# Performance work log

Measured on AMD Instinct MI355X. Metric: run time of the kernel, lower is better.

The kernel has to match this reference:

```python
import jax, jax.numpy as jnp
import numpy as np

L, N, E, H, K = 2048, 8, 2048, 8192, 8

def setup_inputs() -> dict:
    key = jax.random.key(0)
    ks = jax.random.split(key, 6)
    return {
        'x': jax.random.normal(ks[0], (L, N, E), dtype=jnp.float32),
        'proj1': jax.random.normal(ks[1], (H, E), dtype=jnp.float32) * 0.02,
        'proj1_bias': jax.random.normal(ks[2], (H,), dtype=jnp.float32) * 0.02,
        'proj2': jax.random.normal(ks[3], (E, H), dtype=jnp.float32) * 0.02,
        'proj2_bias': jax.random.normal(ks[4], (E,), dtype=jnp.float32) * 0.02,
        'gate_w': jax.random.normal(ks[5], (E, K), dtype=jnp.float32),
    }

def reference(x, proj1, proj1_bias, proj2, proj2_bias, gate_w):
    # Gating: top-1 expert per token (argmax over expert affinities).
    # NOTE: in the source, every expert applies the SAME shared proj1/proj2,
    # and recv_from_experts restores the original token order exactly, so the
    # dispatch/combine is a mathematical identity permutation. The forward
    # math is therefore exactly a shared two-layer GELU MLP on all tokens.
    dst = jnp.argmax(jnp.einsum('lne,ek->lnk', x, gate_w), axis=-1)  # [L,N] int, routing ids
    h = jax.nn.gelu(jnp.einsum('lne,he->lnh', x, proj1) + proj1_bias, approximate=False)
    out = jnp.einsum('lnh,eh->lne', h, proj2) + proj2_bias
    del dst  # routing does not affect the output (shared expert weights)
    return out
```

## Files before the change

### kernel.cpp

```cpp
#include <hip/hip_runtime.h>
#include <hip/hip_bf16.h>
#include <cstdint>
#include <cstddef>

typedef __bf16 bf16_t;
typedef __bf16 bf16x4 __attribute__((ext_vector_type(4)));
typedef __bf16 bf16x8 __attribute__((ext_vector_type(8)));
typedef float  f32x4  __attribute__((ext_vector_type(4)));

#define L_DIM 2048
#define N_DIM 8
#define E_DIM 2048
#define H_DIM 8192
#define T_DIM (L_DIM * N_DIM)

__global__ __launch_bounds__(256) void cvt_f32_bf16(const float* __restrict__ in,
                                                    bf16_t* __restrict__ out,
                                                    int n4) {
    int stride = gridDim.x * blockDim.x;
    for (int i = blockIdx.x * blockDim.x + threadIdx.x; i < n4; i += stride) {
        float4 v = *(const float4*)(in + (size_t)i * 4);
        bf16x4 o;
        o[0] = (bf16_t)v.x; o[1] = (bf16_t)v.y;
        o[2] = (bf16_t)v.z; o[3] = (bf16_t)v.w;
        *(bf16x4*)(out + (size_t)i * 4) = o;
    }
}

__device__ __forceinline__ float fast_gelu(float x) {
    float x2 = x * x;
    float w  = x * __builtin_fmaf(0.1029456f, x2, 2.3022618f);
    w = fminf(w, 60.0f);
    float s = __builtin_amdgcn_exp2f(w);
    float r = __builtin_amdgcn_rcpf(s + 1.0f);
    return x * s * r;
}

template <bool GELU_OUT, int LG_NT, int LG_TN, int LG_NTILE, int KDIM, int NDIM>
__global__ __launch_bounds__(512, 2) void gemm256(const bf16_t* __restrict__ Am,
                                                  const bf16_t* __restrict__ Bm,
                                                  const float* __restrict__ bias,
                                                  void* __restrict__ Cout) {
    extern __shared__ char lds[];
    constexpr int NT    = 1 << LG_NT;
    constexpr int ntile = 1 << LG_NTILE;
    constexpr int U     = ntile << LG_NT;

    const int tid  = threadIdx.x;
    const int lane = tid & 63;
    const int wid  = tid >> 6;
    const int wr   = wid >> 2;
    const int wc   = wid & 3;

    const int wgb = (blockIdx.x & 7) * 32 + (blockIdx.x >> 3);
    const int g0  = wgb << LG_NTILE;

    const int srow  = wid * 8 + (lane >> 3);
    const int scol8 = ((lane & 7) ^ (lane >> 3)) * 8;

    auto STAGE = [&](int isB, int half, int slot) {
        const int us  = (slot < U) ? slot : (U - 1);
        const int ti_ = us >> LG_NT;
        const int kt_ = us & (NT - 1);
        const int g_  = g0 + ti_;
        const size_t base_ = (size_t)(isB ? (g_ & ((1 << LG_TN) - 1)) : (g_ >> LG_TN)) << 8;
        const unsigned reg_ = (unsigned)(((slot & 1) << 16) | (isB << 15) | (half << 14));
        const bf16_t* s0 = (isB ? Bm : Am)
                         + (base_ + (size_t)(half * 128 + srow)) * (size_t)KDIM
                         + (size_t)((kt_ << 6) + scol8);
        __builtin_amdgcn_global_load_lds(
            (const __attribute__((address_space(1))) void*)s0,
            (__attribute__((address_space(3))) void*)(lds + reg_ + (unsigned)(wid * 1024)),
            16, 0, 0);
        __builtin_amdgcn_global_load_lds(
            (const __attribute__((address_space(1))) void*)(s0 + (size_t)64 * KDIM),
            (__attribute__((address_space(3))) void*)(lds + reg_ + (unsigned)((8 + wid) * 1024)),
            16, 0, 0);
    };

    auto ldsA = [&](unsigned bufo, int m, int kk) -> bf16x8 {
        const int row  = (m >> 1) * 64 + wr * 32 + (m & 1) * 16 + (lane & 15);
        const int slot = ((kk << 2) + (lane >> 4)) ^ (lane & 7);
        return *(const bf16x8*)(lds + bufo + row * 128 + slot * 16);
    };
    auto ldsB = [&](unsigned bufo, int n, int kk) -> bf16x8 {
        const int row  = wc * 64 + n * 16 + (lane & 15);
        const int slot = ((kk << 2) + (lane >> 4)) ^ (lane & 7);
        return *(const bf16x8*)(lds + bufo + 32768 + row * 128 + slot * 16);
    };

    f32x4 acc[8][4] = {};

    STAGE(1, 0, 0); STAGE(1, 1, 0); STAGE(0, 0, 0); STAGE(0, 1, 0);
    asm volatile("s_waitcnt vmcnt(0)" ::: "memory");
    __builtin_amdgcn_s_barrier();

    for (int ti = 0; ti < ntile; ++ti) {
        for (int t = 0; t < NT; ++t) {
            const int u = (ti << LG_NT) + t;
            const unsigned cur = (unsigned)(t & 1) * 65536u;
            bf16x8 bf[4][2];
            bf16x8 af[4][2];

            STAGE(1, 0, u + 1);
            STAGE(1, 1, u + 1);
#pragma unroll
            for (int n = 0; n < 4; ++n)
#pragma unroll
                for (int kk = 0; kk < 2; ++kk)
                    bf[n][kk] = ldsB(cur, n, kk);
#pragma unroll
            for (int mm = 0; mm < 4; ++mm)
#pragma unroll
                for (int kk = 0; kk < 2; ++kk)
                    af[mm][kk] = ldsA(cur, mm, kk);
            asm volatile("s_waitcnt vmcnt(4)" ::: "memory");
            __builtin_amdgcn_s_barrier();
            asm volatile("s_waitcnt lgkmcnt(0)" ::: "memory");
            __builtin_amdgcn_s_setprio(1);
#pragma unroll
            for (int mm = 0; mm < 4; ++mm)
#pragma unroll
                for (int n = 0; n < 4; ++n)
#pragma unroll
                    for (int kk = 0; kk < 2; ++kk)
                        acc[mm][n] = __builtin_amdgcn_mfma_f32_16x16x32_bf16(
                            af[mm][kk], bf[n][kk], acc[mm][n], 0, 0, 0);
            __builtin_amdgcn_s_setprio(0);

            STAGE(0, 0, u + 1);
            STAGE(0, 1, u + 1);
#pragma unroll
            for (int mm = 0; mm < 4; ++mm)
#pragma unroll
                for (int kk = 0; kk < 2; ++kk)
                    af[mm][kk] = ldsA(cur, 4 + mm, kk);
            asm volatile("s_waitcnt vmcnt(2)" ::: "memory");
            __builtin_amdgcn_s_barrier();
            asm volatile("s_waitcnt lgkmcnt(0)" ::: "memory");
            __builtin_amdgcn_s_setprio(1);
#pragma unroll
            for (int mm = 0; mm < 4; ++mm)
#pragma unroll
                for (int n = 0; n < 4; ++n)
#pragma unroll
                    for (int kk = 0; kk < 2; ++kk)
                        acc[4 + mm][n] = __builtin_amdgcn_mfma_f32_16x16x32_bf16(
                            af[mm][kk], bf[n][kk], acc[4 + mm][n], 0, 0, 0);
            __builtin_amdgcn_s_setprio(0);
        }

        const int g = g0 + ti;
        const size_t rowBase = (size_t)(g >> LG_TN) << 8;
        const size_t colBase = (size_t)(g & ((1 << LG_TN) - 1)) << 8;
        const int orow = (lane >> 4) * 4;
        const int ocol = lane & 15;
#pragma unroll
        for (int m = 0; m < 8; ++m) {
            const size_t rb = rowBase + (size_t)((m >> 1) * 64 + wr * 32 + (m & 1) * 16 + orow);
#pragma unroll
            for (int n = 0; n < 4; ++n) {
                const size_t col = colBase + (size_t)(wc * 64 + n * 16 + ocol);
                const float bv = bias[col];
#pragma unroll
                for (int j = 0; j < 4; ++j) {
                    float v = acc[m][n][j] + bv;
                    if constexpr (GELU_OUT) {
                        ((bf16_t*)Cout)[(rb + j) * (size_t)NDIM + col] = (bf16_t)fast_gelu(v);
                    } else {
                        ((float*)Cout)[(rb + j) * (size_t)NDIM + col] = v;
                    }
                }
                acc[m][n] = (f32x4){0.f, 0.f, 0.f, 0.f};
            }
        }
    }
    asm volatile("s_waitcnt vmcnt(0)" ::: "memory");
}

extern "C" void kernel_launch(void* const* d_in, const int* in_sizes, int n_in,
                              void* d_out, int out_size, void* d_ws, size_t ws_size,
                              hipStream_t stream) {
    const float* x  = (const float*)d_in[0];
    const float* p1 = (const float*)d_in[1];
    const float* b1 = (const float*)d_in[2];
    const float* p2 = (const float*)d_in[3];
    const float* b2 = (const float*)d_in[4];
    float* out = (float*)d_out;

    char* ws = (char*)d_ws;
    bf16_t* xb  = (bf16_t*)(ws);
    bf16_t* p1b = (bf16_t*)(ws + ((size_t)64 << 20));
    bf16_t* p2b = (bf16_t*)(ws + ((size_t)96 << 20));
    bf16_t* h   = (bf16_t*)(ws + ((size_t)128 << 20));

    auto g1 = gemm256<true, 5, 5, 3, E_DIM, H_DIM>;
    auto g2 = gemm256<false, 7, 3, 1, H_DIM, E_DIM>;

    (void)hipFuncSetAttribute((const void*)g1,
                              hipFuncAttributeMaxDynamicSharedMemorySize, 131072);
    (void)hipFuncSetAttribute((const void*)g2,
                              hipFuncAttributeMaxDynamicSharedMemorySize, 131072);

    cvt_f32_bf16<<<2048, 256, 0, stream>>>(x,  xb,  (T_DIM * E_DIM) / 4);
    cvt_f32_bf16<<<1024, 256, 0, stream>>>(p1, p1b, (H_DIM * E_DIM) / 4);
    cvt_f32_bf16<<<1024, 256, 0, stream>>>(p2, p2b, (E_DIM * H_DIM) / 4);

    g1<<<256, 512, 131072, stream>>>(xb, p1b, b1, (void*)h);
    g2<<<256, 512, 131072, stream>>>(h, p2b, b2, (void*)out);
}
```

Baseline: 1.125 ms.

## Software-pipeline LDS fragment reads across four MFMA sub-phases per k-step

Restructures the GEMM inner loop into four quarter-phases per k-step. Each phase issues one global->LDS stage and prefetches the next A fragments while MFMAs run on the current ones. B fragments and the first A fragments for the next k-step are read from the other LDS buffer ahead of time, using ping-pong register sets, so LDS read latency overlaps compute instead of waiting on lgkmcnt(0). This adds more barriers and more live registers, which risks spills at 2 waves/SIMD. The vmcnt/lgkmcnt waits are fragile for correctness across buffer parity.

```diff
diff --git a/kernel.cpp b/kernel.cpp
--- a/kernel.cpp
+++ b/kernel.cpp
@@ -58,7 +58,7 @@
     const int srow  = wid * 8 + (lane >> 3);
     const int scol8 = ((lane & 7) ^ (lane >> 3)) * 8;
 
-    auto STAGE = [&](int isB, int half, int slot) {
+    auto STAGE_F = [&](int isB, int half, int slot) {
         const int us  = (slot < U) ? slot : (U - 1);
         const int ti_ = us >> LG_NT;
         const int kt_ = us & (NT - 1);
@@ -89,65 +89,76 @@
         return *(const bf16x8*)(lds + bufo + 32768 + row * 128 + slot * 16);
     };
 
-    f32x4 acc[8][4] = {};
-
-    STAGE(1, 0, 0); STAGE(1, 1, 0); STAGE(0, 0, 0); STAGE(0, 1, 0);
+#define RD_A(dst, P, M0) do {                                                   \
+        dst[0][0] = ldsA((P) * 65536u, (M0),     0);                            \
+        dst[0][1] = ldsA((P) * 65536u, (M0),     1);                            \
+        dst[1][0] = ldsA((P) * 65536u, (M0) + 1, 0);                            \
+        dst[1][1] = ldsA((P) * 65536u, (M0) + 1, 1); } while (0)
+#define RD_B(dst, P) do {                                                       \
+        _Pragma("unroll") for (int n_ = 0; n_ < 4; ++n_) {                      \
+            dst[n_][0] = ldsB((P) * 65536u, n_, 0);                             \
+            dst[n_][1] = ldsB((P) * 65536u, n_, 1); } } while (0)
+#define MFMA16(AB, AF, BF) do {                                                 \
+        _Pragma("unroll") for (int mm = 0; mm < 2; ++mm)                        \
+        _Pragma("unroll") for (int n_ = 0; n_ < 4; ++n_)                        \
+        _Pragma("unroll") for (int kk = 0; kk < 2; ++kk)                        \
+            acc[(AB) + mm][n_] = __builtin_amdgcn_mfma_f32_16x16x32_bf16(       \
+                AF[mm][kk], BF[n_][kk], acc[(AB) + mm][n_], 0, 0, 0); } while (0)
+
+#define KITER(U_, PARL, BC, BN) do {                                            \
+        const int u_ = (U_);                                                    \
+                        \
+        STAGE_F(1, 0, u_ + 1);                                                  \
+        RD_A(af_b, PARL, 2);                                                    \
+        asm volatile("s_waitcnt vmcnt(2)" ::: "memory");                        \
+        __builtin_amdgcn_s_barrier();                                           \
+        asm volatile("s_waitcnt lgkmcnt(4)" ::: "memory");                      \
+        __builtin_amdgcn_s_setprio(1);                                          \
+        MFMA16(0, af_a, BC);                                                    \
+        __builtin_amdgcn_s_setprio(0);                                          \
+                        \
+        STAGE_F(1, 1, u_ + 1);                                                  \
+        RD_A(af_a, PARL, 4);                                                    \
+        __builtin_amdgcn_s_barrier();                                           \
+        asm volatile("s_waitcnt lgkmcnt(4)" ::: "memory");                      \
+        __builtin_amdgcn_s_setprio(1);                                          \
+        MFMA16(2, af_b, BC);                                                    \
+        __builtin_amdgcn_s_setprio(0);                                          \
+                        \
+        STAGE_F(0, 0, u_ + 1);                                                  \
+        RD_A(af_b, PARL, 6);                                                    \
+        __builtin_amdgcn_s_barrier();                                           \
+        asm volatile("s_waitcnt lgkmcnt(4)" ::: "memory");                      \
+        __builtin_amdgcn_s_setprio(1);                                          \
+        MFMA16(4, af_a, BC);                                                    \
+        __builtin_amdgcn_s_setprio(0);                                          \
+              \
+                        \
+        STAGE_F(0, 1, u_ + 1);                                                  \
+        asm volatile("s_waitcnt vmcnt(2)" ::: "memory");                        \
+        __builtin_amdgcn_s_barrier();                                           \
+        RD_B(BN, (PARL) ^ 1);                                                   \
+        RD_A(af_a, (PARL) ^ 1, 0);                                              \
+        asm volatile("s_waitcnt lgkmcnt(12)" ::: "memory");                     \
+        __builtin_amdgcn_s_setprio(1);                                          \
+        MFMA16(6, af_b, BC);                                                    \
+        __builtin_amdgcn_s_setprio(0);                                          \
+    } while (0)
+
+    f32x4  acc[8][4] = {};
+    bf16x8 bfP[4][2], bfQ[4][2], af_a[2][2], af_b[2][2];
+
+    STAGE_F(1, 0, 0); STAGE_F(1, 1, 0); STAGE_F(0, 0, 0); STAGE_F(0, 1, 0);
     asm volatile("s_waitcnt vmcnt(0)" ::: "memory");
     __builtin_amdgcn_s_barrier();
+    RD_B(bfP, 0);
+    RD_A(af_a, 0, 0);
 
     for (int ti = 0; ti < ntile; ++ti) {
-        for (int t = 0; t < NT; ++t) {
-            const int u = (ti << LG_NT) + t;
-            const unsigned cur = (unsigned)(t & 1) * 65536u;
-            bf16x8 bf[4][2];
-            bf16x8 af[4][2];
-
-            STAGE(1, 0, u + 1);
-            STAGE(1, 1, u + 1);
-#pragma unroll
-            for (int n = 0; n < 4; ++n)
-#pragma unroll
-                for (int kk = 0; kk < 2; ++kk)
-                    bf[n][kk] = ldsB(cur, n, kk);
-#pragma unroll
-            for (int mm = 0; mm < 4; ++mm)
-#pragma unroll
-                for (int kk = 0; kk < 2; ++kk)
-                    af[mm][kk] = ldsA(cur, mm, kk);
-            asm volatile("s_waitcnt vmcnt(4)" ::: "memory");
-            __builtin_amdgcn_s_barrier();
-            asm volatile("s_waitcnt lgkmcnt(0)" ::: "memory");
-            __builtin_amdgcn_s_setprio(1);
-#pragma unroll
-            for (int mm = 0; mm < 4; ++mm)
-#pragma unroll
-                for (int n = 0; n < 4; ++n)
-#pragma unroll
-                    for (int kk = 0; kk < 2; ++kk)
-                        acc[mm][n] = __builtin_amdgcn_mfma_f32_16x16x32_bf16(
-                            af[mm][kk], bf[n][kk], acc[mm][n], 0, 0, 0);
-            __builtin_amdgcn_s_setprio(0);
-
-            STAGE(0, 0, u + 1);
-            STAGE(0, 1, u + 1);
-#pragma unroll
-            for (int mm = 0; mm < 4; ++mm)
-#pragma unroll
-                for (int kk = 0; kk < 2; ++kk)
-                    af[mm][kk] = ldsA(cur, 4 + mm, kk);
-            asm volatile("s_waitcnt vmcnt(2)" ::: "memory");
-            __builtin_amdgcn_s_barrier();
-            asm volatile("s_waitcnt lgkmcnt(0)" ::: "memory");
-            __builtin_amdgcn_s_setprio(1);
-#pragma unroll
-            for (int mm = 0; mm < 4; ++mm)
-#pragma unroll
-                for (int n = 0; n < 4; ++n)
-#pragma unroll
-                    for (int kk = 0; kk < 2; ++kk)
-                        acc[4 + mm][n] = __builtin_amdgcn_mfma_f32_16x16x32_bf16(
-                            af[mm][kk], bf[n][kk], acc[4 + mm][n], 0, 0, 0);
-            __builtin_amdgcn_s_setprio(0);
+        const int ub = ti << LG_NT;
+        for (int t = 0; t < NT; t += 2) {
+            KITER(ub + t,     0, bfP, bfQ);
+            KITER(ub + t + 1, 1, bfQ, bfP);
         }
 
         const int g = g0 + ti;
@@ -176,6 +187,11 @@
         }
     }
     asm volatile("s_waitcnt vmcnt(0)" ::: "memory");
+
+#undef KITER
+#undef MFMA16
+#undef RD_B
+#undef RD_A
 }
 
 extern "C" void kernel_launch(void* const* d_in, const int* in_sizes, int n_in,
```

Result: slower. 2.783 ms (+147.2%).

## Halve K-tile to 32 and LDS to 64KB, doubling grid with finer MFMA/load interleave

Applied to the files above, without the earlier changes.

Shrinks the K step per stage from 64 to 32 so each stage buffer fits in 64KB of LDS, which allows two workgroups per CU. The grid doubles to 512 blocks, each doing fewer output tiles. The main loop now splits into four barrier-separated phases, each interleaving one global-to-LDS load with a quarter of the MFMAs, and the LDS swizzle is redone for 64-byte rows. The cost is twice as many barriers and pipeline stages per unit of K, with less MFMA work between synchronisation points.

```diff
diff --git a/kernel.cpp b/kernel.cpp
--- a/kernel.cpp
+++ b/kernel.cpp
@@ -52,11 +52,11 @@
     const int wr   = wid >> 2;
     const int wc   = wid & 3;
 
-    const int wgb = (blockIdx.x & 7) * 32 + (blockIdx.x >> 3);
+    const int wgb = (blockIdx.x & 7) * 64 + (blockIdx.x >> 3);
     const int g0  = wgb << LG_NTILE;
 
-    const int srow  = wid * 8 + (lane >> 3);
-    const int scol8 = ((lane & 7) ^ (lane >> 3)) * 8;
+    const int srow  = wid * 16 + (lane >> 2);
+    const int scol8 = ((lane & 3) ^ ((lane >> 3) & 3)) * 8;
 
     auto STAGE = [&](int isB, int half, int slot) {
         const int us  = (slot < U) ? slot : (U - 1);
@@ -64,29 +64,25 @@
         const int kt_ = us & (NT - 1);
         const int g_  = g0 + ti_;
         const size_t base_ = (size_t)(isB ? (g_ & ((1 << LG_TN) - 1)) : (g_ >> LG_TN)) << 8;
-        const unsigned reg_ = (unsigned)(((slot & 1) << 16) | (isB << 15) | (half << 14));
+        const unsigned reg_ = (unsigned)(((slot & 1) << 15) | (isB << 14) | (half << 13));
         const bf16_t* s0 = (isB ? Bm : Am)
                          + (base_ + (size_t)(half * 128 + srow)) * (size_t)KDIM
-                         + (size_t)((kt_ << 6) + scol8);
+                         + (size_t)((kt_ << 5) + scol8);
         __builtin_amdgcn_global_load_lds(
             (const __attribute__((address_space(1))) void*)s0,
             (__attribute__((address_space(3))) void*)(lds + reg_ + (unsigned)(wid * 1024)),
             16, 0, 0);
-        __builtin_amdgcn_global_load_lds(
-            (const __attribute__((address_space(1))) void*)(s0 + (size_t)64 * KDIM),
-            (__attribute__((address_space(3))) void*)(lds + reg_ + (unsigned)((8 + wid) * 1024)),
-            16, 0, 0);
     };
 
-    auto ldsA = [&](unsigned bufo, int m, int kk) -> bf16x8 {
+    auto ldsA = [&](unsigned bufo, int m) -> bf16x8 {
         const int row  = (m >> 1) * 64 + wr * 32 + (m & 1) * 16 + (lane & 15);
-        const int slot = ((kk << 2) + (lane >> 4)) ^ (lane & 7);
-        return *(const bf16x8*)(lds + bufo + row * 128 + slot * 16);
+        const int slot = (lane >> 4) ^ ((row >> 1) & 3);
+        return *(const bf16x8*)(lds + bufo + row * 64 + slot * 16);
     };
-    auto ldsB = [&](unsigned bufo, int n, int kk) -> bf16x8 {
+    auto ldsB = [&](unsigned bufo, int n) -> bf16x8 {
         const int row  = wc * 64 + n * 16 + (lane & 15);
-        const int slot = ((kk << 2) + (lane >> 4)) ^ (lane & 7);
-        return *(const bf16x8*)(lds + bufo + 32768 + row * 128 + slot * 16);
+        const int slot = (lane >> 4) ^ ((row >> 1) & 3);
+        return *(const bf16x8*)(lds + bufo + 16384 + row * 64 + slot * 16);
     };
 
     f32x4 acc[8][4] = {};
@@ -98,55 +94,69 @@
     for (int ti = 0; ti < ntile; ++ti) {
         for (int t = 0; t < NT; ++t) {
             const int u = (ti << LG_NT) + t;
-            const unsigned cur = (unsigned)(t & 1) * 65536u;
-            bf16x8 bf[4][2];
-            bf16x8 af[4][2];
+            const unsigned cur = (unsigned)(t & 1) * 32768u;
+            bf16x8 bf[4];
+            bf16x8 af[2];
 
             STAGE(1, 0, u + 1);
+#pragma unroll
+            for (int n = 0; n < 4; ++n)
+                bf[n] = ldsB(cur, n);
+            af[0] = ldsA(cur, 0);
+            af[1] = ldsA(cur, 1);
+            __builtin_amdgcn_s_barrier();
+            asm volatile("s_waitcnt lgkmcnt(0)" ::: "memory");
+            __builtin_amdgcn_s_setprio(1);
+#pragma unroll
+            for (int mm = 0; mm < 2; ++mm)
+#pragma unroll
+                for (int n = 0; n < 4; ++n)
+                    acc[mm][n] = __builtin_amdgcn_mfma_f32_16x16x32_bf16(
+                        af[mm], bf[n], acc[mm][n], 0, 0, 0);
+            __builtin_amdgcn_s_setprio(0);
+
             STAGE(1, 1, u + 1);
-#pragma unroll
-            for (int n = 0; n < 4; ++n)
-#pragma unroll
-                for (int kk = 0; kk < 2; ++kk)
-                    bf[n][kk] = ldsB(cur, n, kk);
-#pragma unroll
-            for (int mm = 0; mm < 4; ++mm)
-#pragma unroll
-                for (int kk = 0; kk < 2; ++kk)
-                    af[mm][kk] = ldsA(cur, mm, kk);
-            asm volatile("s_waitcnt vmcnt(4)" ::: "memory");
-            __builtin_amdgcn_s_barrier();
-            asm volatile("s_waitcnt lgkmcnt(0)" ::: "memory");
-            __builtin_amdgcn_s_setprio(1);
-#pragma unroll
-            for (int mm = 0; mm < 4; ++mm)
-#pragma unroll
-                for (int n = 0; n < 4; ++n)
-#pragma unroll
-                    for (int kk = 0; kk < 2; ++kk)
-                        acc[mm][n] = __builtin_amdgcn_mfma_f32_16x16x32_bf16(
-                            af[mm][kk], bf[n][kk], acc[mm][n], 0, 0, 0);
+            af[0] = ldsA(cur, 2);
+            af[1] = ldsA(cur, 3);
+            asm volatile("s_waitcnt vmcnt(2)" ::: "memory");
+            __builtin_amdgcn_s_barrier();
+            asm volatile("s_waitcnt lgkmcnt(0)" ::: "memory");
+            __builtin_amdgcn_s_setprio(1);
+#pragma unroll
+            for (int mm = 0; mm < 2; ++mm)
+#pragma unroll
+                for (int n = 0; n < 4; ++n)
+                    acc[2 + mm][n] = __builtin_amdgcn_mfma_f32_16x16x32_bf16(
+                        af[mm], bf[n], acc[2 + mm][n], 0, 0, 0);
             __builtin_amdgcn_s_setprio(0);
 
             STAGE(0, 0, u + 1);
+            af[0] = ldsA(cur, 4);
+            af[1] = ldsA(cur, 5);
+            __builtin_amdgcn_s_barrier();
+            asm volatile("s_waitcnt lgkmcnt(0)" ::: "memory");
+            __builtin_amdgcn_s_setprio(1);
+#pragma unroll
+            for (int mm = 0; mm < 2; ++mm)
+#pragma unroll
+                for (int n = 0; n < 4; ++n)
+                    acc[4 + mm][n] = __builtin_amdgcn_mfma_f32_16x16x32_bf16(
+                        af[mm], bf[n], acc[4 + mm][n], 0, 0, 0);
+            __builtin_amdgcn_s_setprio(0);
+
             STAGE(0, 1, u + 1);
-#pragma unroll
-            for (int mm = 0; mm < 4; ++mm)
-#pragma unroll
-                for (int kk = 0; kk < 2; ++kk)
-                    af[mm][kk] = ldsA(cur, 4 + mm, kk);
-            asm volatile("s_waitcnt vmcnt(2)" ::: "memory");
-            __builtin_amdgcn_s_barrier();
-            asm volatile("s_waitcnt lgkmcnt(0)" ::: "memory");
-            __builtin_amdgcn_s_setprio(1);
-#pragma unroll
-            for (int mm = 0; mm < 4; ++mm)
-#pragma unroll
-                for (int n = 0; n < 4; ++n)
-#pragma unroll
-                    for (int kk = 0; kk < 2; ++kk)
-                        acc[4 + mm][n] = __builtin_amdgcn_mfma_f32_16x16x32_bf16(
-                            af[mm][kk], bf[n][kk], acc[4 + mm][n], 0, 0, 0);
+            af[0] = ldsA(cur, 6);
+            af[1] = ldsA(cur, 7);
+            asm volatile("s_waitcnt vmcnt(1)" ::: "memory");
+            __builtin_amdgcn_s_barrier();
+            asm volatile("s_waitcnt lgkmcnt(0)" ::: "memory");
+            __builtin_amdgcn_s_setprio(1);
+#pragma unroll
+            for (int mm = 0; mm < 2; ++mm)
+#pragma unroll
+                for (int n = 0; n < 4; ++n)
+                    acc[6 + mm][n] = __builtin_amdgcn_mfma_f32_16x16x32_bf16(
+                        af[mm], bf[n], acc[6 + mm][n], 0, 0, 0);
             __builtin_amdgcn_s_setprio(0);
         }
 
@@ -194,18 +204,18 @@
     bf16_t* p2b = (bf16_t*)(ws + ((size_t)96 << 20));
     bf16_t* h   = (bf16_t*)(ws + ((size_t)128 << 20));
 
-    auto g1 = gemm256<true, 5, 5, 3, E_DIM, H_DIM>;
-    auto g2 = gemm256<false, 7, 3, 1, H_DIM, E_DIM>;
+    auto g1 = gemm256<true, 6, 5, 2, E_DIM, H_DIM>;
+    auto g2 = gemm256<false, 8, 3, 0, H_DIM, E_DIM>;
 
     (void)hipFuncSetAttribute((const void*)g1,
-                              hipFuncAttributeMaxDynamicSharedMemorySize, 131072);
+                              hipFuncAttributeMaxDynamicSharedMemorySize, 65536);
     (void)hipFuncSetAttribute((const void*)g2,
-                              hipFuncAttributeMaxDynamicSharedMemorySize, 131072);
+                              hipFuncAttributeMaxDynamicSharedMemorySize, 65536);
 
     cvt_f32_bf16<<<2048, 256, 0, stream>>>(x,  xb,  (T_DIM * E_DIM) / 4);
     cvt_f32_bf16<<<1024, 256, 0, stream>>>(p1, p1b, (H_DIM * E_DIM) / 4);
     cvt_f32_bf16<<<1024, 256, 0, stream>>>(p2, p2b, (E_DIM * H_DIM) / 4);
 
-    g1<<<256, 512, 131072, stream>>>(xb, p1b, b1, (void*)h);
-    g2<<<256, 512, 131072, stream>>>(h, p2b, b2, (void*)out);
-}
+    g1<<<512, 512, 65536, stream>>>(xb, p1b, b1, (void*)h);
+    g2<<<512, 512, 65536, stream>>>(h, p2b, b2, (void*)out);
+}
```

Measured after the change: 1.124 ms. No clear change (-0.1%).
